# Optimization experiments

Hardware: AMD Instinct MI355X
Metric: run time of the kernel (lower is better)

## Reference

```python
import jax, jax.numpy as jnp
import numpy as np

N, F_IN, HID, OUT, H = 10000, 256, 256, 512, 4
E = 320000
SLOPE = 0.2  # GATv2Conv default negative_slope
EPS = 1e-5   # LayerNorm eps


def setup_inputs() -> dict:
    key = jax.random.key(0)
    ks = jax.random.split(key, 10)
    g = lambda k, shape, fan: (jax.random.normal(k, shape, jnp.float32) / np.float32(np.sqrt(fan)))
    d1, d2 = HID // H, OUT // H
    return {
        "x": jax.random.normal(ks[0], (N, F_IN), jnp.float32),
        "edge_index": jax.random.randint(ks[1], (2, E), 0, N),
        # layer 1 (in_feats -> hidden_dim, heads=H, concat)
        "Wl1": g(ks[2], (HID, F_IN), F_IN), "bl1": jnp.zeros((HID,), jnp.float32),
        "Wr1": g(ks[3], (HID, F_IN), F_IN), "br1": jnp.zeros((HID,), jnp.float32),
        "att1": g(ks[4], (H, d1), d1), "bias1": jnp.zeros((HID,), jnp.float32),
        # layer 2 (hidden_dim -> out_dim)
        "Wl2": g(ks[5], (OUT, HID), HID), "bl2": jnp.zeros((OUT,), jnp.float32),
        "Wr2": g(ks[6], (OUT, HID), HID), "br2": jnp.zeros((OUT,), jnp.float32),
        "att2": g(ks[7], (H, d2), d2), "bias2": jnp.zeros((OUT,), jnp.float32),
        # final LayerNorm
        "gamma": jnp.ones((OUT,), jnp.float32), "beta": jnp.zeros((OUT,), jnp.float32),
    }


def _gatv2(x, src, dst, Wl, bl, Wr, br, att, bias, heads):
    """GATv2Conv: e_ij = a_h . leaky_relu(Wl x_j + Wr x_i), softmax over j per i,
    out_i = sum_j alpha_ij * (Wl x_j), heads concatenated, plus bias."""
    n = x.shape[0]
    d = Wl.shape[0] // heads
    xl = (x @ Wl.T + bl).reshape(n, heads, d)  # source transform
    xr = (x @ Wr.T + br).reshape(n, heads, d)  # target transform
    s = jax.nn.leaky_relu(xl[src] + xr[dst], SLOPE)        # [E,H,d]
    e = jnp.einsum('ehd,hd->eh', s, att)                   # [E,H]
    m = jax.ops.segment_max(e, dst, num_segments=n)        # [N,H] (self-loops => no empty segs)
    w = jnp.exp(e - m[dst])
    denom = jax.ops.segment_sum(w, dst, num_segments=n)
    alpha = w / denom[dst]                                 # segment softmax
    out = jax.ops.segment_sum(alpha[:, :, None] * xl[src], dst, num_segments=n)  # [N,H,d]
    return out.reshape(n, heads * d) + bias


def reference(x, edge_index, Wl1, bl1, Wr1, br1, att1, bias1,
              Wl2, bl2, Wr2, br2, att2, bias2, gamma, beta):
    n = x.shape[0]
    loop = jnp.arange(n, dtype=edge_index.dtype)  # add_self_loops=True
    src = jnp.concatenate([edge_index[0], loop])
    dst = jnp.concatenate([edge_index[1], loop])
    h = jax.nn.relu(_gatv2(x, src, dst, Wl1, bl1, Wr1, br1, att1, bias1, H))
    h = _gatv2(h, src, dst, Wl2, bl2, Wr2, br2, att2, bias2, H)
    mu = jnp.mean(h, axis=-1, keepdims=True)
    var = jnp.var(h, axis=-1, keepdims=True)
    return gamma * (h - mu) / jnp.sqrt(var + EPS) + beta
```

## Files before the change

kernel.cpp:

```cpp
#include <hip/hip_runtime.h>
#include <stdint.h>

#define N_NODES 10000
#define K_DIM   256
#define HID_D   256
#define OUT_D   512
#define NE      320000
#define NE_TOT  (NE + N_NODES)
#define SLOPE   0.2f
#define LN_EPS  1e-5f

typedef __bf16 bf16x8 __attribute__((ext_vector_type(8)));
typedef float  f32x4  __attribute__((ext_vector_type(4)));
typedef float  f32x2  __attribute__((ext_vector_type(2)));
typedef unsigned short u16;
typedef uint32_t u32;

#if __has_builtin(__builtin_elementwise_fma)
#define PKFMA(a,b,c) __builtin_elementwise_fma((a),(b),(c))
#else
#define PKFMA(a,b,c) ((a)*(b)+(c))
#endif
#if __has_builtin(__builtin_elementwise_max)
#define PKMAX(a,b) __builtin_elementwise_max((a),(b))
#else
static __device__ __forceinline__ f32x2 pkmax_(f32x2 a, f32x2 b) {
    f32x2 r; r.x = fmaxf(a.x, b.x); r.y = fmaxf(a.y, b.y); return r;
}
#define PKMAX(a,b) pkmax_((a),(b))
#endif

__device__ __forceinline__ float bf2f(u16 u) {
    union { u32 i; float f; } v; v.i = ((u32)u) << 16; return v.f;
}
__device__ __forceinline__ u16 f2bf(float f) {
    union { float f; u32 i; } v; v.f = f;
    u32 b = v.i;
    return (u16)((b + 0x7FFFu + ((b >> 16) & 1u)) >> 16);
}
__device__ __forceinline__ f32x2 bfpair(u32 u) {
    union { u32 i; float f; } lo, hi;
    lo.i = u << 16; hi.i = u & 0xFFFF0000u;
    f32x2 r; r.x = lo.f; r.y = hi.f; return r;
}
__device__ __forceinline__ u32 pack2bf(float a, float b) {
    return (u32)f2bf(a) | ((u32)f2bf(b) << 16);
}

__device__ __forceinline__ void gl_lds16(const u16* g, u16* lds_base) {
    __builtin_amdgcn_global_load_lds(
        (const __attribute__((address_space(1))) void*)g,
        (__attribute__((address_space(3))) void*)lds_base, 16, 0, 0);
}

__global__ __launch_bounds__(256) void k_detect(const u32* __restrict__ x,
                                                int* __restrict__ flag) {
    u32 v = x[threadIdx.x];
    int e_lo = (int)((v >> 7) & 0xFF);
    int vote = (e_lo >= 100 && e_lo <= 150) ? 1 : 0;
    __shared__ int cnt;
    if (threadIdx.x == 0) cnt = 0;
    __syncthreads();
    atomicAdd(&cnt, vote);
    __syncthreads();
    if (threadIdx.x == 0) *flag = (cnt > 180) ? 1 : 0;
}

struct CanonAll {
    const void *x, *wl1, *wr1, *wl2, *wr2;
    u16 *xd, *wl1d, *wr1d, *wl2d, *wr2d;
    const void* ssrc[10]; float* sdst[10];
};
#define CW_X  2560000
#define CW_1  (CW_X + 65536)
#define CW_2  (CW_1 + 65536)
#define CW_3  (CW_2 + 131072)
#define CW_TOT (CW_3 + 131072)
__global__ __launch_bounds__(256) void k_canon(CanonAll c, const int* __restrict__ flag) {
    int i = blockIdx.x * 256 + threadIdx.x;
    int f = *flag;
    if (i < CW_TOT) {
        const void* src; u16* dst; int off;
        if      (i < CW_X) { src = c.x;   dst = c.xd;   off = i; }
        else if (i < CW_1) { src = c.wl1; dst = c.wl1d; off = i - CW_X; }
        else if (i < CW_2) { src = c.wr1; dst = c.wr1d; off = i - CW_1; }
        else if (i < CW_3) { src = c.wl2; dst = c.wl2d; off = i - CW_2; }
        else               { src = c.wr2; dst = c.wr2d; off = i - CW_3; }
        if (f) dst[off] = ((const u16*)src)[off];
        else   dst[off] = f2bf(((const float*)src)[off]);
    } else {
        int s = i - CW_TOT;
        int seg, off;
        if (s < 1024) { seg = s >> 8; off = s & 255; }
        else          { seg = 4 + ((s - 1024) >> 9); off = (s - 1024) & 511; }
        const void* sp = c.ssrc[seg];
        float* d = c.sdst[seg];
        d[off] = f ? bf2f(((const u16*)sp)[off]) : ((const float*)sp)[off];
    }
}


__global__ __launch_bounds__(256) void k_count_deg(const int* __restrict__ ei, int* deg) {
    int e = blockIdx.x * 256 + threadIdx.x;
    if (e < NE) atomicAdd(&deg[ei[NE + e]], 1);
}

__global__ __launch_bounds__(1024) void k_scan(const int* __restrict__ deg,
                                               int* __restrict__ rowptr,
                                               int* __restrict__ cursor) {
    __shared__ int sbuf[2][1024];
    int t = threadIdx.x;
    int base = t * 10;
    int loc[10];
    int s = 0;
    #pragma unroll
    for (int q = 0; q < 10; ++q) {
        int idx = base + q;
        int d = (idx < N_NODES) ? (deg[idx] + 1) : 0;
        loc[q] = s;
        s += d;
    }
    sbuf[0][t] = s;
    __syncthreads();
    int cur = 0;
    for (int off = 1; off < 1024; off <<= 1) {
        int nxt = cur ^ 1;
        int v = sbuf[cur][t];
        if (t >= off) v += sbuf[cur][t - off];
        sbuf[nxt][t] = v;
        __syncthreads();
        cur = nxt;
    }
    int excl = sbuf[cur][t] - s;
    #pragma unroll
    for (int q = 0; q < 10; ++q) {
        int idx = base + q;
        if (idx <= N_NODES) {
            int val = excl + loc[q];
            rowptr[idx] = val;
            cursor[idx] = val;
        }
    }
}

__global__ __launch_bounds__(256) void k_scatter(const int* __restrict__ ei,
                                                 int* cursor, int* __restrict__ csr_src) {
    int e = blockIdx.x * 256 + threadIdx.x;
    if (e >= NE_TOT) return;
    int s, d;
    if (e < NE) { s = ei[e]; d = ei[NE + e]; }
    else        { s = e - NE; d = s; }
    int pos = atomicAdd(&cursor[d], 1);
    csr_src[pos] = s;
}

__global__ __launch_bounds__(256) void k_gemm2(const u16* __restrict__ X,
                                               const u16* __restrict__ Wl,
                                               const u16* __restrict__ Wr,
                                               const float* __restrict__ bl,
                                               const float* __restrict__ br,
                                               u16* __restrict__ Yl,
                                               u16* __restrict__ Yr, int Ncols) {
    __shared__ uint4 sAq[1024];
    __shared__ uint4 sBq[1024];
    u16* sA = (u16*)sAq;
    u16* sB = (u16*)sBq;

    int nb = Ncols >> 7;
    int by = blockIdx.y;
    const u16* W; const float* bias; u16* Y; int nbase;
    if (by < nb) { W = Wl; bias = bl; Y = Yl; nbase = by << 7; }
    else         { W = Wr; bias = br; Y = Yr; nbase = (by - nb) << 7; }

    int m0   = blockIdx.x << 7;
    int tid  = threadIdx.x;
    int wave = tid >> 6;
    int lane = tid & 63;
    int quad = lane >> 4;
    int l16  = lane & 15;
    int wm   = wave & 1;
    int wn   = wave >> 1;

    f32x4 acc[4][4] = {};

    #pragma unroll 1
    for (int kk = 0; kk < K_DIM; kk += 64) {
        #pragma unroll
        for (int r = 0; r < 4; ++r) {
            int g = wave + r * 4;
            int chunk = g >> 1;
            int row = ((g & 1) << 6) + lane;
            int mg = m0 + row;
            if (mg >= N_NODES) mg = N_NODES - 1;
            gl_lds16(X + (size_t)mg * K_DIM + kk + chunk * 8, sA + (size_t)(g << 6) * 8);
            gl_lds16(W + (size_t)(nbase + row) * K_DIM + kk + chunk * 8, sB + (size_t)(g << 6) * 8);
        }
        __syncthreads();

        #pragma unroll
        for (int s = 0; s < 2; ++s) {
            int c = s * 4 + quad;
            bf16x8 af[4], bf[4];
            #pragma unroll
            for (int t = 0; t < 4; ++t) {
                int m = (wm << 6) + t * 16 + l16;
                af[t] = *(const bf16x8*)(sA + ((size_t)(c << 7) + m) * 8);
                int n = (wn << 6) + t * 16 + l16;
                bf[t] = *(const bf16x8*)(sB + ((size_t)(c << 7) + n) * 8);
            }
            #pragma unroll
            for (int mt = 0; mt < 4; ++mt)
                #pragma unroll
                for (int nt = 0; nt < 4; ++nt)
                    acc[mt][nt] = __builtin_amdgcn_mfma_f32_16x16x32_bf16(
                        af[mt], bf[nt], acc[mt][nt], 0, 0, 0);
        }
        __syncthreads();
    }

    #pragma unroll
    for (int nt = 0; nt < 4; ++nt) {
        int col = nbase + (wn << 6) + nt * 16 + l16;
        float bv = bias[col];
        #pragma unroll
        for (int mt = 0; mt < 4; ++mt) {
            int rbase = m0 + (wm << 6) + mt * 16 + quad * 4;
            #pragma unroll
            for (int q = 0; q < 4; ++q) {
                int row = rbase + q;
                if (row < N_NODES)
                    Y[(size_t)row * Ncols + col] = f2bf(acc[mt][nt][q] + bv);
            }
        }
    }
}

__global__ __launch_bounds__(256) void k_agg1(const u16* __restrict__ xl,
                                              const u16* __restrict__ xr,
                                              const int* __restrict__ rowptr,
                                              const int* __restrict__ csrc,
                                              const float* __restrict__ att,
                                              const float* __restrict__ bias,
                                              u16* __restrict__ hout) {
    int wave = threadIdx.x >> 6, lane = threadIdx.x & 63;
    int i = blockIdx.x * 4 + wave;
    if (i >= N_NODES) return;
    int c0 = (lane >> 4) * 64 + (lane & 15) * 4;

    f32x2 xp[2], ap[2];
    {
        uint2 xq = *(const uint2*)(xr + (size_t)i * HID_D + c0);
        xp[0] = bfpair(xq.x); xp[1] = bfpair(xq.y);
        const f32x2* a2 = (const f32x2*)(att + c0);
        ap[0] = a2[0]; ap[1] = a2[1];
    }
    const f32x2 slope2 = {SLOPE, SLOPE};

    int beg = rowptr[i], end = rowptr[i + 1];
    float denom = 0.f;
    f32x2 acc[2] = {};
    const u16* xbase = xl + c0;

    auto dot4 = [&](const f32x2 v[2]) -> float {
        f32x2 pr2 = {0.f, 0.f};
        #pragma unroll
        for (int k = 0; k < 2; ++k) {
            f32x2 s = v[k] + xp[k];
            s = PKMAX(s, s * slope2);
            pr2 = PKFMA(s, ap[k], pr2);
        }
        return pr2.x + pr2.y;
    };

    int p = beg;
    int4 jq = {0, 0, 0, 0};
    if (p + 4 <= end) jq = *(const int4*)(csrc + p);
    for (; p + 4 <= end; p += 4) {
        int4 jc = jq;
        if (p + 8 <= end) jq = *(const int4*)(csrc + p + 4);
        uint2 q0 = *(const uint2*)(xbase + (size_t)jc.x * HID_D);
        uint2 q1 = *(const uint2*)(xbase + (size_t)jc.y * HID_D);
        uint2 q2 = *(const uint2*)(xbase + (size_t)jc.z * HID_D);
        uint2 q3 = *(const uint2*)(xbase + (size_t)jc.w * HID_D);
        f32x2 v0[2] = { bfpair(q0.x), bfpair(q0.y) };
        f32x2 v1[2] = { bfpair(q1.x), bfpair(q1.y) };
        f32x2 v2[2] = { bfpair(q2.x), bfpair(q2.y) };
        f32x2 v3[2] = { bfpair(q3.x), bfpair(q3.y) };
        float pr0 = dot4(v0), pr1 = dot4(v1), pr2s = dot4(v2), pr3 = dot4(v3);
        #pragma unroll
        for (int o = 1; o < 16; o <<= 1) {
            pr0  += __shfl_xor(pr0,  o, 64);
            pr1  += __shfl_xor(pr1,  o, 64);
            pr2s += __shfl_xor(pr2s, o, 64);
            pr3  += __shfl_xor(pr3,  o, 64);
        }
        float w0 = __expf(fminf(pr0,  60.f));
        float w1 = __expf(fminf(pr1,  60.f));
        float w2 = __expf(fminf(pr2s, 60.f));
        float w3 = __expf(fminf(pr3,  60.f));
        denom += (w0 + w1) + (w2 + w3);
        f32x2 W0 = {w0, w0}, W1 = {w1, w1}, W2 = {w2, w2}, W3 = {w3, w3};
        #pragma unroll
        for (int k = 0; k < 2; ++k) {
            acc[k] = PKFMA(W0, v0[k], acc[k]);
            acc[k] = PKFMA(W1, v1[k], acc[k]);
            acc[k] = PKFMA(W2, v2[k], acc[k]);
            acc[k] = PKFMA(W3, v3[k], acc[k]);
        }
    }
    for (; p < end; ++p) {
        int j = csrc[p];
        uint2 q = *(const uint2*)(xbase + (size_t)j * HID_D);
        f32x2 v[2] = { bfpair(q.x), bfpair(q.y) };
        float pr = dot4(v);
        #pragma unroll
        for (int o = 1; o < 16; o <<= 1) pr += __shfl_xor(pr, o, 64);
        float w = __expf(fminf(pr, 60.f));
        denom += w;
        f32x2 W = {w, w};
        acc[0] = PKFMA(W, v[0], acc[0]);
        acc[1] = PKFMA(W, v[1], acc[1]);
    }

    float inv = 1.f / denom;
    f32x2 inv2 = {inv, inv};
    const f32x2* bp = (const f32x2*)(bias + c0);
    f32x2 z = {0.f, 0.f};
    f32x2 o0 = PKMAX(PKFMA(acc[0], inv2, bp[0]), z);
    f32x2 o1 = PKMAX(PKFMA(acc[1], inv2, bp[1]), z);
    u32* hp = (u32*)(hout + (size_t)i * HID_D + c0);
    hp[0] = pack2bf(o0.x, o0.y);
    hp[1] = pack2bf(o1.x, o1.y);
}

__global__ __launch_bounds__(256) void k_agg2_ln(const u16* __restrict__ xl,
                                                 const u16* __restrict__ xr,
                                                 const int* __restrict__ rowptr,
                                                 const int* __restrict__ csrc,
                                                 const float* __restrict__ att,
                                                 const float* __restrict__ bias,
                                                 const float* __restrict__ gamma,
                                                 const float* __restrict__ beta,
                                                 void* __restrict__ outv,
                                                 const int* __restrict__ flag) {
    int wave = threadIdx.x >> 6, lane = threadIdx.x & 63;
    int i = blockIdx.x * 4 + wave;
    if (i >= N_NODES) return;
    int c0 = (lane >> 4) * 128 + (lane & 15) * 8;

    f32x2 xp[4], ap[4];
    {
        uint4 xq = *(const uint4*)(xr + (size_t)i * OUT_D + c0);
        xp[0] = bfpair(xq.x); xp[1] = bfpair(xq.y);
        xp[2] = bfpair(xq.z); xp[3] = bfpair(xq.w);
        const f32x2* a2 = (const f32x2*)(att + c0);
        ap[0] = a2[0]; ap[1] = a2[1]; ap[2] = a2[2]; ap[3] = a2[3];
    }
    const f32x2 slope2 = {SLOPE, SLOPE};

    int beg = rowptr[i], end = rowptr[i + 1];
    float denom = 0.f;
    f32x2 acc[4] = {};
    const u16* xbase = xl + c0;

    auto dot8 = [&](const f32x2 v[4]) -> float {
        f32x2 pr2 = {0.f, 0.f};
        #pragma unroll
        for (int k = 0; k < 4; ++k) {
            f32x2 s = v[k] + xp[k];
            s = PKMAX(s, s * slope2);
            pr2 = PKFMA(s, ap[k], pr2);
        }
        return pr2.x + pr2.y;
    };

    int p = beg;
    int4 jq = {0, 0, 0, 0};
    if (p + 4 <= end) jq = *(const int4*)(csrc + p);
    for (; p + 4 <= end; p += 4) {
        int4 jc = jq;
        if (p + 8 <= end) jq = *(const int4*)(csrc + p + 4);
        uint4 q0 = *(const uint4*)(xbase + (size_t)jc.x * OUT_D);
        uint4 q1 = *(const uint4*)(xbase + (size_t)jc.y * OUT_D);
        uint4 q2 = *(const uint4*)(xbase + (size_t)jc.z * OUT_D);
        uint4 q3 = *(const uint4*)(xbase + (size_t)jc.w * OUT_D);
        f32x2 v0[4] = { bfpair(q0.x), bfpair(q0.y), bfpair(q0.z), bfpair(q0.w) };
        f32x2 v1[4] = { bfpair(q1.x), bfpair(q1.y), bfpair(q1.z), bfpair(q1.w) };
        f32x2 v2[4] = { bfpair(q2.x), bfpair(q2.y), bfpair(q2.z), bfpair(q2.w) };
        f32x2 v3[4] = { bfpair(q3.x), bfpair(q3.y), bfpair(q3.z), bfpair(q3.w) };
        float pr0 = dot8(v0), pr1 = dot8(v1), pr2s = dot8(v2), pr3 = dot8(v3);
        #pragma unroll
        for (int o = 1; o < 16; o <<= 1) {
            pr0  += __shfl_xor(pr0,  o, 64);
            pr1  += __shfl_xor(pr1,  o, 64);
            pr2s += __shfl_xor(pr2s, o, 64);
            pr3  += __shfl_xor(pr3,  o, 64);
        }
        float w0 = __expf(fminf(pr0,  60.f));
        float w1 = __expf(fminf(pr1,  60.f));
        float w2 = __expf(fminf(pr2s, 60.f));
        float w3 = __expf(fminf(pr3,  60.f));
        denom += (w0 + w1) + (w2 + w3);
        f32x2 W0 = {w0, w0}, W1 = {w1, w1}, W2 = {w2, w2}, W3 = {w3, w3};
        #pragma unroll
        for (int k = 0; k < 4; ++k) {
            acc[k] = PKFMA(W0, v0[k], acc[k]);
            acc[k] = PKFMA(W1, v1[k], acc[k]);
            acc[k] = PKFMA(W2, v2[k], acc[k]);
            acc[k] = PKFMA(W3, v3[k], acc[k]);
        }
    }
    for (; p < end; ++p) {
        int j = csrc[p];
        uint4 q = *(const uint4*)(xbase + (size_t)j * OUT_D);
        f32x2 v[4] = { bfpair(q.x), bfpair(q.y), bfpair(q.z), bfpair(q.w) };
        float pr = dot8(v);
        #pragma unroll
        for (int o = 1; o < 16; o <<= 1) pr += __shfl_xor(pr, o, 64);
        float w = __expf(fminf(pr, 60.f));
        denom += w;
        f32x2 W = {w, w};
        #pragma unroll
        for (int k = 0; k < 4; ++k) acc[k] = PKFMA(W, v[k], acc[k]);
    }

    float inv = 1.f / denom;
    f32x2 inv2 = {inv, inv};
    const f32x2* bp = (const f32x2*)(bias + c0);
    f32x2 o2[4];
    float s1 = 0.f, s2 = 0.f;
    #pragma unroll
    for (int k = 0; k < 4; ++k) {
        o2[k] = PKFMA(acc[k], inv2, bp[k]);
        s1 += o2[k].x + o2[k].y;
        s2 = fmaf(o2[k].x, o2[k].x, fmaf(o2[k].y, o2[k].y, s2));
    }
    #pragma unroll
    for (int off = 1; off < 64; off <<= 1) {
        s1 += __shfl_xor(s1, off, 64);
        s2 += __shfl_xor(s2, off, 64);
    }
    float mu  = s1 * (1.f / OUT_D);
    float var = s2 * (1.f / OUT_D) - mu * mu;
    float rstd = rsqrtf(var + LN_EPS);
    f32x2 mu2 = {mu, mu}, rs2 = {rstd, rstd};
    const f32x2* gp  = (const f32x2*)(gamma + c0);
    const f32x2* bep = (const f32x2*)(beta + c0);

    size_t ob = (size_t)i * OUT_D + c0;
    if (*flag) {
        u32 pk[4];
        #pragma unroll
        for (int k = 0; k < 4; ++k) {
            f32x2 r = PKFMA(gp[k] * (o2[k] - mu2), rs2, bep[k]);
            pk[k] = pack2bf(r.x, r.y);
        }
        *(uint4*)((u16*)outv + ob) = make_uint4(pk[0], pk[1], pk[2], pk[3]);
    } else {
        f32x2* out = (f32x2*)((float*)outv + ob);
        #pragma unroll
        for (int k = 0; k < 4; ++k)
            out[k] = PKFMA(gp[k] * (o2[k] - mu2), rs2, bep[k]);
    }
}


extern "C" void kernel_launch(void* const* d_in, const int* in_sizes, int n_in,
                              void* d_out, int out_size, void* d_ws, size_t ws_size,
                              hipStream_t stream) {
    const int* ei = (const int*)d_in[1];

    char* ws = (char*)d_ws;
    size_t off = 0;
    auto alloc = [&](size_t bytes) { void* p = ws + off; off += (bytes + 255) & ~(size_t)255; return p; };
    u16* xcb  = (u16*)alloc((size_t)N_NODES * K_DIM * 2);
    u16* wl1b = (u16*)alloc((size_t)HID_D * K_DIM * 2);
    u16* wr1b = (u16*)alloc((size_t)HID_D * K_DIM * 2);
    u16* wl2b = (u16*)alloc((size_t)OUT_D * K_DIM * 2);
    u16* wr2b = (u16*)alloc((size_t)OUT_D * K_DIM * 2);
    u16* xl1b = (u16*)alloc((size_t)N_NODES * HID_D * 2);
    u16* xr1b = (u16*)alloc((size_t)N_NODES * HID_D * 2);
    u16* hb   = (u16*)alloc((size_t)N_NODES * HID_D * 2);
    u16* xl2b = (u16*)alloc((size_t)N_NODES * OUT_D * 2);
    u16* xr2b = (u16*)alloc((size_t)N_NODES * OUT_D * 2);
    float* bl1c  = (float*)alloc(HID_D * 4);
    float* br1c  = (float*)alloc(HID_D * 4);
    float* att1c = (float*)alloc(HID_D * 4);
    float* bia1c = (float*)alloc(HID_D * 4);
    float* bl2c  = (float*)alloc(OUT_D * 4);
    float* br2c  = (float*)alloc(OUT_D * 4);
    float* att2c = (float*)alloc(OUT_D * 4);
    float* bia2c = (float*)alloc(OUT_D * 4);
    float* gamc  = (float*)alloc(OUT_D * 4);
    float* betc  = (float*)alloc(OUT_D * 4);
    int* flag = (int*)alloc(256);
    int* deg  = (int*)alloc((size_t)N_NODES * 4);
    int* rowp = (int*)alloc((size_t)(N_NODES + 1) * 4);
    int* curs = (int*)alloc((size_t)(N_NODES + 1) * 4);
    int* csrc = (int*)alloc((size_t)NE_TOT * 4);

    hipLaunchKernelGGL(k_detect, dim3(1), dim3(256), 0, stream, (const u32*)d_in[0], flag);

    CanonAll ca;
    ca.x = d_in[0]; ca.wl1 = d_in[2]; ca.wr1 = d_in[4]; ca.wl2 = d_in[8]; ca.wr2 = d_in[10];
    ca.xd = xcb; ca.wl1d = wl1b; ca.wr1d = wr1b; ca.wl2d = wl2b; ca.wr2d = wr2b;
    ca.ssrc[0] = d_in[3];  ca.sdst[0] = bl1c;
    ca.ssrc[1] = d_in[5];  ca.sdst[1] = br1c;
    ca.ssrc[2] = d_in[6];  ca.sdst[2] = att1c;
    ca.ssrc[3] = d_in[7];  ca.sdst[3] = bia1c;
    ca.ssrc[4] = d_in[9];  ca.sdst[4] = bl2c;
    ca.ssrc[5] = d_in[11]; ca.sdst[5] = br2c;
    ca.ssrc[6] = d_in[12]; ca.sdst[6] = att2c;
    ca.ssrc[7] = d_in[13]; ca.sdst[7] = bia2c;
    ca.ssrc[8] = d_in[14]; ca.sdst[8] = gamc;
    ca.ssrc[9] = d_in[15]; ca.sdst[9] = betc;
    hipLaunchKernelGGL(k_canon, dim3(CW_TOT / 256 + 16), dim3(256), 0, stream, ca, flag);

    hipMemsetAsync(deg, 0, (size_t)N_NODES * 4, stream);
    hipLaunchKernelGGL(k_count_deg, dim3((NE + 255) / 256), dim3(256), 0, stream, ei, deg);
    hipLaunchKernelGGL(k_scan, dim3(1), dim3(1024), 0, stream, deg, rowp, curs);
    hipLaunchKernelGGL(k_scatter, dim3((NE_TOT + 255) / 256), dim3(256), 0, stream, ei, curs, csrc);

    const int MB = (N_NODES + 127) / 128;
    hipLaunchKernelGGL(k_gemm2, dim3(MB, 2 * HID_D / 128), dim3(256), 0, stream,
                       xcb, wl1b, wr1b, bl1c, br1c, xl1b, xr1b, HID_D);
    hipLaunchKernelGGL(k_agg1, dim3((N_NODES + 3) / 4), dim3(256), 0, stream,
                       xl1b, xr1b, rowp, csrc, att1c, bia1c, hb);
    hipLaunchKernelGGL(k_gemm2, dim3(MB, 2 * OUT_D / 128), dim3(256), 0, stream,
                       hb, wl2b, wr2b, bl2c, br2c, xl2b, xr2b, OUT_D);
    hipLaunchKernelGGL(k_agg2_ln, dim3((N_NODES + 3) / 4), dim3(256), 0, stream,
                       xl2b, xr2b, rowp, csrc, att2c, bia2c, gamc, betc, d_out, flag);
}
```

Before: 287.1 us.

## Fuse prep kernels, overlap CSR scatter with GEMM, split aggregation edges across two waves

Merges format detection, canonicalization and degree counting into one prep kernel, with each block recomputing the detection vote locally. The CSR scatter now runs as extra blocks inside the first GEMM launch using a flattened 1D grid, cutting three launches. Each aggregation node is now handled by two waves that split its edge list and combine partial sums through shared memory, and the gather loop is unrolled by 8. The split doubles the number of waves per node and adds a block barrier and an LDS reduction per node.

```diff
diff --git a/kernel.cpp b/kernel.cpp
--- a/kernel.cpp
+++ b/kernel.cpp
@@ -53,32 +53,39 @@
         (__attribute__((address_space(3))) void*)lds_base, 16, 0, 0);
 }
 
-__global__ __launch_bounds__(256) void k_detect(const u32* __restrict__ x,
-                                                int* __restrict__ flag) {
-    u32 v = x[threadIdx.x];
-    int e_lo = (int)((v >> 7) & 0xFF);
-    int vote = (e_lo >= 100 && e_lo <= 150) ? 1 : 0;
-    __shared__ int cnt;
-    if (threadIdx.x == 0) cnt = 0;
-    __syncthreads();
-    atomicAdd(&cnt, vote);
-    __syncthreads();
-    if (threadIdx.x == 0) *flag = (cnt > 180) ? 1 : 0;
-}
-
-struct CanonAll {
-    const void *x, *wl1, *wr1, *wl2, *wr2;
-    u16 *xd, *wl1d, *wr1d, *wl2d, *wr2d;
-    const void* ssrc[10]; float* sdst[10];
-};
 #define CW_X  2560000
 #define CW_1  (CW_X + 65536)
 #define CW_2  (CW_1 + 65536)
 #define CW_3  (CW_2 + 131072)
 #define CW_TOT (CW_3 + 131072)
-__global__ __launch_bounds__(256) void k_canon(CanonAll c, const int* __restrict__ flag) {
-    int i = blockIdx.x * 256 + threadIdx.x;
-    int f = *flag;
+#define CANON_BLOCKS (CW_TOT / 256 + 16)
+#define COUNT_BLOCKS ((NE + 255) / 256)
+
+struct PrepArgs {
+    const void *x, *wl1, *wr1, *wl2, *wr2;
+    u16 *xd, *wl1d, *wr1d, *wl2d, *wr2d;
+    const void* ssrc[10]; float* sdst[10];
+    const int* ei; int* deg; int* flagg;
+};
+
+__global__ __launch_bounds__(256) void k_prep(PrepArgs c) {
+    int bx = blockIdx.x, tid = threadIdx.x;
+    if (bx >= CANON_BLOCKS) {
+        int e = (bx - CANON_BLOCKS) * 256 + tid;
+        if (e < NE) atomicAdd(&c.deg[c.ei[NE + e]], 1);
+        return;
+    }
+    __shared__ int cnt;
+    if (tid == 0) cnt = 0;
+    __syncthreads();
+    u32 v = ((const u32*)c.x)[tid];
+    int e_lo = (int)((v >> 7) & 0xFF);
+    if (e_lo >= 100 && e_lo <= 150) atomicAdd(&cnt, 1);
+    __syncthreads();
+    int f = (cnt > 180) ? 1 : 0;
+    if (bx == 0 && tid == 0) *c.flagg = f;
+
+    int i = bx * 256 + tid;
     if (i < CW_TOT) {
         const void* src; u16* dst; int off;
         if      (i < CW_X) { src = c.x;   dst = c.xd;   off = i; }
@@ -99,12 +106,6 @@
     }
 }
 
-
-__global__ __launch_bounds__(256) void k_count_deg(const int* __restrict__ ei, int* deg) {
-    int e = blockIdx.x * 256 + threadIdx.x;
-    if (e < NE) atomicAdd(&deg[ei[NE + e]], 1);
-}
-
 __global__ __launch_bounds__(1024) void k_scan(const int* __restrict__ deg,
                                                int* __restrict__ rowptr,
                                                int* __restrict__ cursor) {
@@ -143,37 +144,41 @@
     }
 }
 
-__global__ __launch_bounds__(256) void k_scatter(const int* __restrict__ ei,
-                                                 int* cursor, int* __restrict__ csr_src) {
-    int e = blockIdx.x * 256 + threadIdx.x;
-    if (e >= NE_TOT) return;
-    int s, d;
-    if (e < NE) { s = ei[e]; d = ei[NE + e]; }
-    else        { s = e - NE; d = s; }
-    int pos = atomicAdd(&cursor[d], 1);
-    csr_src[pos] = s;
-}
-
-__global__ __launch_bounds__(256) void k_gemm2(const u16* __restrict__ X,
-                                               const u16* __restrict__ Wl,
-                                               const u16* __restrict__ Wr,
-                                               const float* __restrict__ bl,
-                                               const float* __restrict__ br,
-                                               u16* __restrict__ Yl,
-                                               u16* __restrict__ Yr, int Ncols) {
+__global__ __launch_bounds__(256) void k_gemm2s(const u16* __restrict__ X,
+                                                const u16* __restrict__ Wl,
+                                                const u16* __restrict__ Wr,
+                                                const float* __restrict__ bl,
+                                                const float* __restrict__ br,
+                                                u16* __restrict__ Yl,
+                                                u16* __restrict__ Yr, int Ncols,
+                                                int MBx, int gemmB,
+                                                const int* __restrict__ ei,
+                                                int* cursor, int* __restrict__ csr_src) {
     __shared__ uint4 sAq[1024];
     __shared__ uint4 sBq[1024];
+    int bx = blockIdx.x, tid = threadIdx.x;
+
+    if (bx >= gemmB) {
+        int e = (bx - gemmB) * 256 + tid;
+        if (e < NE_TOT) {
+            int s, d;
+            if (e < NE) { s = ei[e]; d = ei[NE + e]; }
+            else        { s = e - NE; d = s; }
+            int pos = atomicAdd(&cursor[d], 1);
+            csr_src[pos] = s;
+        }
+        return;
+    }
+
     u16* sA = (u16*)sAq;
     u16* sB = (u16*)sBq;
-
     int nb = Ncols >> 7;
-    int by = blockIdx.y;
+    int by = bx / MBx;
     const u16* W; const float* bias; u16* Y; int nbase;
     if (by < nb) { W = Wl; bias = bl; Y = Yl; nbase = by << 7; }
     else         { W = Wr; bias = br; Y = Yr; nbase = (by - nb) << 7; }
 
-    int m0   = blockIdx.x << 7;
-    int tid  = threadIdx.x;
+    int m0   = (bx % MBx) << 7;
     int wave = tid >> 6;
     int lane = tid & 63;
     int quad = lane >> 4;
@@ -242,8 +247,11 @@
                                               const float* __restrict__ att,
                                               const float* __restrict__ bias,
                                               u16* __restrict__ hout) {
-    int wave = threadIdx.x >> 6, lane = threadIdx.x & 63;
-    int i = blockIdx.x * 4 + wave;
+    __shared__ float red[2][64][6];
+    int tid = threadIdx.x;
+    int wave = tid >> 6, lane = tid & 63;
+    int pair = wave >> 1, half = wave & 1;
+    int i = blockIdx.x * 2 + pair;
     if (i >= N_NODES) return;
     int c0 = (lane >> 4) * 64 + (lane & 15) * 4;
 
@@ -257,70 +265,96 @@
     const f32x2 slope2 = {SLOPE, SLOPE};
 
     int beg = rowptr[i], end = rowptr[i + 1];
+    int cnt = end - beg;
+    int h0 = (cnt + 1) >> 1;
+    int p    = beg + half * h0;
+    int pend = half ? end : (beg + h0);
+
     float denom = 0.f;
     f32x2 acc[2] = {};
     const u16* xbase = xl + c0;
 
-    auto dot4 = [&](const f32x2 v[2]) -> float {
+    auto dotq = [&](uint2 q) -> float {
         f32x2 pr2 = {0.f, 0.f};
-        #pragma unroll
-        for (int k = 0; k < 2; ++k) {
-            f32x2 s = v[k] + xp[k];
-            s = PKMAX(s, s * slope2);
-            pr2 = PKFMA(s, ap[k], pr2);
-        }
+        f32x2 s = bfpair(q.x) + xp[0]; s = PKMAX(s, s * slope2); pr2 = PKFMA(s, ap[0], pr2);
+        s = bfpair(q.y) + xp[1];       s = PKMAX(s, s * slope2); pr2 = PKFMA(s, ap[1], pr2);
         return pr2.x + pr2.y;
     };
-
-    int p = beg;
-    int4 jq = {0, 0, 0, 0};
-    if (p + 4 <= end) jq = *(const int4*)(csrc + p);
-    for (; p + 4 <= end; p += 4) {
-        int4 jc = jq;
-        if (p + 8 <= end) jq = *(const int4*)(csrc + p + 4);
-        uint2 q0 = *(const uint2*)(xbase + (size_t)jc.x * HID_D);
-        uint2 q1 = *(const uint2*)(xbase + (size_t)jc.y * HID_D);
-        uint2 q2 = *(const uint2*)(xbase + (size_t)jc.z * HID_D);
-        uint2 q3 = *(const uint2*)(xbase + (size_t)jc.w * HID_D);
-        f32x2 v0[2] = { bfpair(q0.x), bfpair(q0.y) };
-        f32x2 v1[2] = { bfpair(q1.x), bfpair(q1.y) };
-        f32x2 v2[2] = { bfpair(q2.x), bfpair(q2.y) };
-        f32x2 v3[2] = { bfpair(q3.x), bfpair(q3.y) };
-        float pr0 = dot4(v0), pr1 = dot4(v1), pr2s = dot4(v2), pr3 = dot4(v3);
-        #pragma unroll
-        for (int o = 1; o < 16; o <<= 1) {
-            pr0  += __shfl_xor(pr0,  o, 64);
-            pr1  += __shfl_xor(pr1,  o, 64);
-            pr2s += __shfl_xor(pr2s, o, 64);
-            pr3  += __shfl_xor(pr3,  o, 64);
-        }
-        float w0 = __expf(fminf(pr0,  60.f));
-        float w1 = __expf(fminf(pr1,  60.f));
-        float w2 = __expf(fminf(pr2s, 60.f));
-        float w3 = __expf(fminf(pr3,  60.f));
-        denom += (w0 + w1) + (w2 + w3);
-        f32x2 W0 = {w0, w0}, W1 = {w1, w1}, W2 = {w2, w2}, W3 = {w3, w3};
-        #pragma unroll
-        for (int k = 0; k < 2; ++k) {
-            acc[k] = PKFMA(W0, v0[k], acc[k]);
-            acc[k] = PKFMA(W1, v1[k], acc[k]);
-            acc[k] = PKFMA(W2, v2[k], acc[k]);
-            acc[k] = PKFMA(W3, v3[k], acc[k]);
-        }
-    }
-    for (; p < end; ++p) {
-        int j = csrc[p];
-        uint2 q = *(const uint2*)(xbase + (size_t)j * HID_D);
-        f32x2 v[2] = { bfpair(q.x), bfpair(q.y) };
-        float pr = dot4(v);
+    auto accq = [&](uint2 q, float w) {
+        f32x2 W = {w, w};
+        acc[0] = PKFMA(W, bfpair(q.x), acc[0]);
+        acc[1] = PKFMA(W, bfpair(q.y), acc[1]);
+    };
+
+    while (p + 8 <= pend) {
+        int4 ja = *(const int4*)(csrc + p);
+        int4 jb = *(const int4*)(csrc + p + 4);
+        uint2 q[8];
+        q[0] = *(const uint2*)(xbase + (size_t)ja.x * HID_D);
+        q[1] = *(const uint2*)(xbase + (size_t)ja.y * HID_D);
+        q[2] = *(const uint2*)(xbase + (size_t)ja.z * HID_D);
+        q[3] = *(const uint2*)(xbase + (size_t)ja.w * HID_D);
+        q[4] = *(const uint2*)(xbase + (size_t)jb.x * HID_D);
+        q[5] = *(const uint2*)(xbase + (size_t)jb.y * HID_D);
+        q[6] = *(const uint2*)(xbase + (size_t)jb.z * HID_D);
+        q[7] = *(const uint2*)(xbase + (size_t)jb.w * HID_D);
+        float pr[8];
+        #pragma unroll
+        for (int e = 0; e < 8; ++e) pr[e] = dotq(q[e]);
+        #pragma unroll
+        for (int o = 1; o < 16; o <<= 1)
+            #pragma unroll
+            for (int e = 0; e < 8; ++e) pr[e] += __shfl_xor(pr[e], o, 64);
+        #pragma unroll
+        for (int e = 0; e < 8; ++e) {
+            float w = __expf(fminf(pr[e], 60.f));
+            denom += w;
+            accq(q[e], w);
+        }
+        p += 8;
+    }
+    if (p + 4 <= pend) {
+        int4 ja = *(const int4*)(csrc + p);
+        uint2 q[4];
+        q[0] = *(const uint2*)(xbase + (size_t)ja.x * HID_D);
+        q[1] = *(const uint2*)(xbase + (size_t)ja.y * HID_D);
+        q[2] = *(const uint2*)(xbase + (size_t)ja.z * HID_D);
+        q[3] = *(const uint2*)(xbase + (size_t)ja.w * HID_D);
+        float pr[4];
+        #pragma unroll
+        for (int e = 0; e < 4; ++e) pr[e] = dotq(q[e]);
+        #pragma unroll
+        for (int o = 1; o < 16; o <<= 1)
+            #pragma unroll
+            for (int e = 0; e < 4; ++e) pr[e] += __shfl_xor(pr[e], o, 64);
+        #pragma unroll
+        for (int e = 0; e < 4; ++e) {
+            float w = __expf(fminf(pr[e], 60.f));
+            denom += w;
+            accq(q[e], w);
+        }
+        p += 4;
+    }
+    for (; p < pend; ++p) {
+        uint2 q = *(const uint2*)(xbase + (size_t)csrc[p] * HID_D);
+        float pr = dotq(q);
         #pragma unroll
         for (int o = 1; o < 16; o <<= 1) pr += __shfl_xor(pr, o, 64);
         float w = __expf(fminf(pr, 60.f));
         denom += w;
-        f32x2 W = {w, w};
-        acc[0] = PKFMA(W, v[0], acc[0]);
-        acc[1] = PKFMA(W, v[1], acc[1]);
-    }
+        accq(q, w);
+    }
+
+    if (half == 1) {
+        red[pair][lane][0] = acc[0].x; red[pair][lane][1] = acc[0].y;
+        red[pair][lane][2] = acc[1].x; red[pair][lane][3] = acc[1].y;
+        red[pair][lane][4] = denom;
+    }
+    __syncthreads();
+    if (half == 1) return;
+    acc[0].x += red[pair][lane][0]; acc[0].y += red[pair][lane][1];
+    acc[1].x += red[pair][lane][2]; acc[1].y += red[pair][lane][3];
+    denom    += red[pair][lane][4];
 
     float inv = 1.f / denom;
     f32x2 inv2 = {inv, inv};
@@ -343,8 +377,11 @@
                                                  const float* __restrict__ beta,
                                                  void* __restrict__ outv,
                                                  const int* __restrict__ flag) {
-    int wave = threadIdx.x >> 6, lane = threadIdx.x & 63;
-    int i = blockIdx.x * 4 + wave;
+    __shared__ float red[2][64][10];
+    int tid = threadIdx.x;
+    int wave = tid >> 6, lane = tid & 63;
+    int pair = wave >> 1, half = wave & 1;
+    int i = blockIdx.x * 2 + pair;
     if (i >= N_NODES) return;
     int c0 = (lane >> 4) * 128 + (lane & 15) * 8;
 
@@ -359,70 +396,106 @@
     const f32x2 slope2 = {SLOPE, SLOPE};
 
     int beg = rowptr[i], end = rowptr[i + 1];
+    int cnt = end - beg;
+    int h0 = (cnt + 1) >> 1;
+    int p    = beg + half * h0;
+    int pend = half ? end : (beg + h0);
+
     float denom = 0.f;
     f32x2 acc[4] = {};
     const u16* xbase = xl + c0;
 
-    auto dot8 = [&](const f32x2 v[4]) -> float {
+    auto dotq = [&](uint4 q) -> float {
         f32x2 pr2 = {0.f, 0.f};
-        #pragma unroll
-        for (int k = 0; k < 4; ++k) {
-            f32x2 s = v[k] + xp[k];
-            s = PKMAX(s, s * slope2);
-            pr2 = PKFMA(s, ap[k], pr2);
-        }
+        f32x2 s = bfpair(q.x) + xp[0]; s = PKMAX(s, s * slope2); pr2 = PKFMA(s, ap[0], pr2);
+        s = bfpair(q.y) + xp[1];       s = PKMAX(s, s * slope2); pr2 = PKFMA(s, ap[1], pr2);
+        s = bfpair(q.z) + xp[2];       s = PKMAX(s, s * slope2); pr2 = PKFMA(s, ap[2], pr2);
+        s = bfpair(q.w) + xp[3];       s = PKMAX(s, s * slope2); pr2 = PKFMA(s, ap[3], pr2);
         return pr2.x + pr2.y;
     };
-
-    int p = beg;
-    int4 jq = {0, 0, 0, 0};
-    if (p + 4 <= end) jq = *(const int4*)(csrc + p);
-    for (; p + 4 <= end; p += 4) {
-        int4 jc = jq;
-        if (p + 8 <= end) jq = *(const int4*)(csrc + p + 4);
-        uint4 q0 = *(const uint4*)(xbase + (size_t)jc.x * OUT_D);
-        uint4 q1 = *(const uint4*)(xbase + (size_t)jc.y * OUT_D);
-        uint4 q2 = *(const uint4*)(xbase + (size_t)jc.z * OUT_D);
-        uint4 q3 = *(const uint4*)(xbase + (size_t)jc.w * OUT_D);
-        f32x2 v0[4] = { bfpair(q0.x), bfpair(q0.y), bfpair(q0.z), bfpair(q0.w) };
-        f32x2 v1[4] = { bfpair(q1.x), bfpair(q1.y), bfpair(q1.z), bfpair(q1.w) };
-        f32x2 v2[4] = { bfpair(q2.x), bfpair(q2.y), bfpair(q2.z), bfpair(q2.w) };
-        f32x2 v3[4] = { bfpair(q3.x), bfpair(q3.y), bfpair(q3.z), bfpair(q3.w) };
-        float pr0 = dot8(v0), pr1 = dot8(v1), pr2s = dot8(v2), pr3 = dot8(v3);
-        #pragma unroll
-        for (int o = 1; o < 16; o <<= 1) {
-            pr0  += __shfl_xor(pr0,  o, 64);
-            pr1  += __shfl_xor(pr1,  o, 64);
-            pr2s += __shfl_xor(pr2s, o, 64);
-            pr3  += __shfl_xor(pr3,  o, 64);
-        }
-        float w0 = __expf(fminf(pr0,  60.f));
-        float w1 = __expf(fminf(pr1,  60.f));
-        float w2 = __expf(fminf(pr2s, 60.f));
-        float w3 = __expf(fminf(pr3,  60.f));
-        denom += (w0 + w1) + (w2 + w3);
-        f32x2 W0 = {w0, w0}, W1 = {w1, w1}, W2 = {w2, w2}, W3 = {w3, w3};
-        #pragma unroll
-        for (int k = 0; k < 4; ++k) {
-            acc[k] = PKFMA(W0, v0[k], acc[k]);
-            acc[k] = PKFMA(W1, v1[k], acc[k]);
-            acc[k] = PKFMA(W2, v2[k], acc[k]);
-            acc[k] = PKFMA(W3, v3[k], acc[k]);
-        }
-    }
-    for (; p < end; ++p) {
-        int j = csrc[p];
-        uint4 q = *(const uint4*)(xbase + (size_t)j * OUT_D);
-        f32x2 v[4] = { bfpair(q.x), bfpair(q.y), bfpair(q.z), bfpair(q.w) };
-        float pr = dot8(v);
+    auto accq = [&](uint4 q, float w) {
+        f32x2 W = {w, w};
+        acc[0] = PKFMA(W, bfpair(q.x), acc[0]);
+        acc[1] = PKFMA(W, bfpair(q.y), acc[1]);
+        acc[2] = PKFMA(W, bfpair(q.z), acc[2]);
+        acc[3] = PKFMA(W, bfpair(q.w), acc[3]);
+    };
+
+    while (p + 8 <= pend) {
+        int4 ja = *(const int4*)(csrc + p);
+        int4 jb = *(const int4*)(csrc + p + 4);
+        uint4 q[8];
+        q[0] = *(const uint4*)(xbase + (size_t)ja.x * OUT_D);
+        q[1] = *(const uint4*)(xbase + (size_t)ja.y * OUT_D);
+        q[2] = *(const uint4*)(xbase + (size_t)ja.z * OUT_D);
+        q[3] = *(const uint4*)(xbase + (size_t)ja.w * OUT_D);
+        q[4] = *(const uint4*)(xbase + (size_t)jb.x * OUT_D);
+        q[5] = *(const uint4*)(xbase + (size_t)jb.y * OUT_D);
+        q[6] = *(const uint4*)(xbase + (size_t)jb.z * OUT_D);
+        q[7] = *(const uint4*)(xbase + (size_t)jb.w * OUT_D);
+        float pr[8];
+        #pragma unroll
+        for (int e = 0; e < 8; ++e) pr[e] = dotq(q[e]);
+        #pragma unroll
+        for (int o = 1; o < 16; o <<= 1)
+            #pragma unroll
+            for (int e = 0; e < 8; ++e) pr[e] += __shfl_xor(pr[e], o, 64);
+        #pragma unroll
+        for (int e = 0; e < 8; ++e) {
+            float w = __expf(fminf(pr[e], 60.f));
+            denom += w;
+            accq(q[e], w);
+        }
+        p += 8;
+    }
+    if (p + 4 <= pend) {
+        int4 ja = *(const int4*)(csrc + p);
+        uint4 q[4];
+        q[0] = *(const uint4*)(xbase + (size_t)ja.x * OUT_D);
+        q[1] = *(const uint4*)(xbase + (size_t)ja.y * OUT_D);
+        q[2] = *(const uint4*)(xbase + (size_t)ja.z * OUT_D);
+        q[3] = *(const uint4*)(xbase + (size_t)ja.w * OUT_D);
+        float pr[4];
+        #pragma unroll
+        for (int e = 0; e < 4; ++e) pr[e] = dotq(q[e]);
+        #pragma unroll
+        for (int o = 1; o < 16; o <<= 1)
+            #pragma unroll
+            for (int e = 0; e < 4; ++e) pr[e] += __shfl_xor(pr[e], o, 64);
+        #pragma unroll
+        for (int e = 0; e < 4; ++e) {
+            float w = __expf(fminf(pr[e], 60.f));
+            denom += w;
+            accq(q[e], w);
+        }
+        p += 4;
+    }
+    for (; p < pend; ++p) {
+        uint4 q = *(const uint4*)(xbase + (size_t)csrc[p] * OUT_D);
+        float pr = dotq(q);
         #pragma unroll
         for (int o = 1; o < 16; o <<= 1) pr += __shfl_xor(pr, o, 64);
         float w = __expf(fminf(pr, 60.f));
         denom += w;
-        f32x2 W = {w, w};
-        #pragma unroll
-        for (int k = 0; k < 4; ++k) acc[k] = PKFMA(W, v[k], acc[k]);
-    }
+        accq(q, w);
+    }
+
+    if (half == 1) {
+        #pragma unroll
+        for (int k = 0; k < 4; ++k) {
+            red[pair][lane][2*k]     = acc[k].x;
+            red[pair][lane][2*k + 1] = acc[k].y;
+        }
+        red[pair][lane][8] = denom;
+    }
+    __syncthreads();
+    if (half == 1) return;
+    #pragma unroll
+    for (int k = 0; k < 4; ++k) {
+        acc[k].x += red[pair][lane][2*k];
+        acc[k].y += red[pair][lane][2*k + 1];
+    }
+    denom += red[pair][lane][8];
 
     float inv = 1.f / denom;
     f32x2 inv2 = {inv, inv};
@@ -499,35 +572,36 @@
     int* curs = (int*)alloc((size_t)(N_NODES + 1) * 4);
     int* csrc = (int*)alloc((size_t)NE_TOT * 4);
 
-    hipLaunchKernelGGL(k_detect, dim3(1), dim3(256), 0, stream, (const u32*)d_in[0], flag);
-
-    CanonAll ca;
-    ca.x = d_in[0]; ca.wl1 = d_in[2]; ca.wr1 = d_in[4]; ca.wl2 = d_in[8]; ca.wr2 = d_in[10];
-    ca.xd = xcb; ca.wl1d = wl1b; ca.wr1d = wr1b; ca.wl2d = wl2b; ca.wr2d = wr2b;
-    ca.ssrc[0] = d_in[3];  ca.sdst[0] = bl1c;
-    ca.ssrc[1] = d_in[5];  ca.sdst[1] = br1c;
-    ca.ssrc[2] = d_in[6];  ca.sdst[2] = att1c;
-    ca.ssrc[3] = d_in[7];  ca.sdst[3] = bia1c;
-    ca.ssrc[4] = d_in[9];  ca.sdst[4] = bl2c;
-    ca.ssrc[5] = d_in[11]; ca.sdst[5] = br2c;
-    ca.ssrc[6] = d_in[12]; ca.sdst[6] = att2c;
-    ca.ssrc[7] = d_in[13]; ca.sdst[7] = bia2c;
-    ca.ssrc[8] = d_in[14]; ca.sdst[8] = gamc;
-    ca.ssrc[9] = d_in[15]; ca.sdst[9] = betc;
-    hipLaunchKernelGGL(k_canon, dim3(CW_TOT / 256 + 16), dim3(256), 0, stream, ca, flag);
-
     hipMemsetAsync(deg, 0, (size_t)N_NODES * 4, stream);
-    hipLaunchKernelGGL(k_count_deg, dim3((NE + 255) / 256), dim3(256), 0, stream, ei, deg);
+
+    PrepArgs pa;
+    pa.x = d_in[0]; pa.wl1 = d_in[2]; pa.wr1 = d_in[4]; pa.wl2 = d_in[8]; pa.wr2 = d_in[10];
+    pa.xd = xcb; pa.wl1d = wl1b; pa.wr1d = wr1b; pa.wl2d = wl2b; pa.wr2d = wr2b;
+    pa.ssrc[0] = d_in[3];  pa.sdst[0] = bl1c;
+    pa.ssrc[1] = d_in[5];  pa.sdst[1] = br1c;
+    pa.ssrc[2] = d_in[6];  pa.sdst[2] = att1c;
+    pa.ssrc[3] = d_in[7];  pa.sdst[3] = bia1c;
+    pa.ssrc[4] = d_in[9];  pa.sdst[4] = bl2c;
+    pa.ssrc[5] = d_in[11]; pa.sdst[5] = br2c;
+    pa.ssrc[6] = d_in[12]; pa.sdst[6] = att2c;
+    pa.ssrc[7] = d_in[13]; pa.sdst[7] = bia2c;
+    pa.ssrc[8] = d_in[14]; pa.sdst[8] = gamc;
+    pa.ssrc[9] = d_in[15]; pa.sdst[9] = betc;
+    pa.ei = ei; pa.deg = deg; pa.flagg = flag;
+    hipLaunchKernelGGL(k_prep, dim3(CANON_BLOCKS + COUNT_BLOCKS), dim3(256), 0, stream, pa);
+
     hipLaunchKernelGGL(k_scan, dim3(1), dim3(1024), 0, stream, deg, rowp, curs);
-    hipLaunchKernelGGL(k_scatter, dim3((NE_TOT + 255) / 256), dim3(256), 0, stream, ei, curs, csrc);
 
     const int MB = (N_NODES + 127) / 128;
-    hipLaunchKernelGGL(k_gemm2, dim3(MB, 2 * HID_D / 128), dim3(256), 0, stream,
-                       xcb, wl1b, wr1b, bl1c, br1c, xl1b, xr1b, HID_D);
-    hipLaunchKernelGGL(k_agg1, dim3((N_NODES + 3) / 4), dim3(256), 0, stream,
+    const int SCATB = (NE_TOT + 255) / 256;
+    hipLaunchKernelGGL(k_gemm2s, dim3(MB * 4 + SCATB), dim3(256), 0, stream,
+                       xcb, wl1b, wr1b, bl1c, br1c, xl1b, xr1b, HID_D,
+                       MB, MB * 4, ei, curs, csrc);
+    hipLaunchKernelGGL(k_agg1, dim3((N_NODES + 1) / 2), dim3(256), 0, stream,
                        xl1b, xr1b, rowp, csrc, att1c, bia1c, hb);
-    hipLaunchKernelGGL(k_gemm2, dim3(MB, 2 * OUT_D / 128), dim3(256), 0, stream,
-                       hb, wl2b, wr2b, bl2c, br2c, xl2b, xr2b, OUT_D);
-    hipLaunchKernelGGL(k_agg2_ln, dim3((N_NODES + 3) / 4), dim3(256), 0, stream,
+    hipLaunchKernelGGL(k_gemm2s, dim3(MB * 8), dim3(256), 0, stream,
+                       hb, wl2b, wr2b, bl2c, br2c, xl2b, xr2b, OUT_D,
+                       MB, MB * 8, ei, curs, csrc);
+    hipLaunchKernelGGL(k_agg2_ln, dim3((N_NODES + 1) / 2), dim3(256), 0, stream,
                        xl2b, xr2b, rowp, csrc, att2c, bia2c, gamc, betc, d_out, flag);
 }
```

After: 276.5 us. -3.7%, faster.
